# Kernel optimization log

Hardware: AMD Instinct MI355X
Metric: run time of the kernel (lower is better)

The kernel has to match this reference:

```python
import jax, jax.numpy as jnp
import numpy as np

B, N, C, H = 1, 4096, 768, 12
HD = C // H  # 64
EPS = 1e-5


def _rope_freqs(n, hd, theta=10000.0):
    inv = 1.0 / (theta ** (np.arange(0, hd, 2, dtype=np.float32) / hd))  # (hd/2,)
    ang = np.outer(np.arange(n, dtype=np.float32), inv)  # (N, hd/2)
    return jnp.asarray(np.cos(ang)), jnp.asarray(np.sin(ang))


def setup_inputs() -> dict:
    key = jax.random.key(0)
    ks = jax.random.split(key, 5)
    cos, sin = _rope_freqs(N, HD)
    s = lambda d: 1.0 / np.sqrt(d)
    return {
        "x": jax.random.normal(ks[0], (B, N, C), jnp.float32),
        "freqs_cos": cos,
        "freqs_sin": sin,
        "w_qkv": jax.random.normal(ks[1], (3 * C, C), jnp.float32) * s(C),
        "w_proj": jax.random.normal(ks[2], (C, C), jnp.float32) * s(C),
        "b_proj": jnp.zeros((C,), jnp.float32),
        "g1": jnp.ones((C,), jnp.float32),
        "beta1": jnp.zeros((C,), jnp.float32),
        "g2": jnp.ones((C,), jnp.float32),
        "beta2": jnp.zeros((C,), jnp.float32),
        "w_fc1": jax.random.normal(ks[3], (4 * C, C), jnp.float32) * s(C),
        "b_fc1": jnp.zeros((4 * C,), jnp.float32),
        "w_fc2": jax.random.normal(ks[4], (C, 4 * C), jnp.float32) * s(4 * C),
        "b_fc2": jnp.zeros((C,), jnp.float32),
    }


def _layernorm(x, g, b):
    mu = jnp.mean(x, -1, keepdims=True)
    var = jnp.mean(jnp.square(x - mu), -1, keepdims=True)
    return (x - mu) * jax.lax.rsqrt(var + EPS) * g + b


def _apply_rope(t, cos, sin):
    # t: (B, N, H, HD); cos/sin: (N, HD/2) -> broadcast (1, N, 1, HD/2)
    t = t.reshape(*t.shape[:-1], HD // 2, 2)
    t0, t1 = t[..., 0], t[..., 1]
    c = cos[None, :, None, :]
    s = sin[None, :, None, :]
    out = jnp.stack([t0 * c - t1 * s, t0 * s + t1 * c], axis=-1)
    return out.reshape(*out.shape[:-2], HD)


def reference(x, freqs_cos, freqs_sin, w_qkv, w_proj, b_proj, g1, beta1, g2, beta2,
              w_fc1, b_fc1, w_fc2, b_fc2):
    # --- attention branch ---
    h = _layernorm(x, g1, beta1)
    qkv = (h @ w_qkv.T).reshape(B, N, 3, H, HD)
    q, k, v = qkv[:, :, 0], qkv[:, :, 1], qkv[:, :, 2]  # (B,N,H,HD)
    q = _apply_rope(q, freqs_cos, freqs_sin)
    k = _apply_rope(k, freqs_cos, freqs_sin)
    scale = HD ** (-0.5)
    attn = jnp.einsum('bnhd,bmhd->bhnm', q, k) * scale
    attn = jax.nn.softmax(attn, axis=-1)
    o = jnp.einsum('bhnm,bmhd->bnhd', attn, v).reshape(B, N, C)
    x = x + o @ w_proj.T + b_proj
    # --- mlp branch ---
    h = _layernorm(x, g2, beta2)
    h = jax.nn.gelu(h @ w_fc1.T + b_fc1, approximate=False)
    x = x + h @ w_fc2.T + b_fc2
    return x
```

## Files before the change

kernel.cpp:

```cpp
#include <hip/hip_runtime.h>
#include <hip/hip_bf16.h>
#include <math.h>

#define LOG2E 1.44269504088896340736f

typedef short bf16x8 __attribute__((ext_vector_type(8)));
typedef float f32x4 __attribute__((ext_vector_type(4)));

static __device__ __forceinline__ float bf2f(ushort u){
  union { float f; unsigned int u; } x; x.u = ((unsigned int)u) << 16; return x.f;
}
static __device__ __forceinline__ ushort f2bf(float f){
  union { float f; unsigned int u; } x; x.f = f;
  unsigned int r = x.u + 0x7fffu + ((x.u >> 16) & 1u);
  return (ushort)(r >> 16);
}
static __device__ __forceinline__ unsigned cvt_pk_bf16(float a, float b){
  unsigned r;
  asm("v_cvt_pk_bf16_f32 %0, %1, %2" : "=v"(r) : "v"(a), "v"(b));
  return r;
}
static __device__ __forceinline__ float fmax3(float a, float b, float c){
  return fmaxf(fmaxf(a, b), c);
}
static __device__ __forceinline__ float dpp_xor1(float v){
  int i = __builtin_amdgcn_mov_dpp(__float_as_int(v), 0xB1, 0xF, 0xF, true);
  return __int_as_float(i);
}
static __device__ __forceinline__ void gload_lds16(const void* g, void* l){
  __builtin_amdgcn_global_load_lds(
      (const __attribute__((address_space(1))) unsigned int*)g,
      (__attribute__((address_space(3))) unsigned int*)l, 16, 0, 0);
}

__global__ __launch_bounds__(256) void cvt_all(const float* __restrict__ s0, ushort* __restrict__ d0, int c0,
                                               const float* __restrict__ s1, ushort* __restrict__ d1, int c1,
                                               const float* __restrict__ s2, ushort* __restrict__ d2, int c2,
                                               const float* __restrict__ s3, ushort* __restrict__ d3, int c3){
  int j = blockIdx.x * 256 + threadIdx.x;
  const float* s; ushort* d;
  if (j < c0){ s = s0; d = d0; }
  else { j -= c0;
    if (j < c1){ s = s1; d = d1; }
    else { j -= c1;
      if (j < c2){ s = s2; d = d2; }
      else { j -= c2; if (j >= c3) return; s = s3; d = d3; } } }
  float4 v = ((const float4*)s)[j];
  ushort4 o;
  o.x = f2bf(v.x); o.y = f2bf(v.y); o.z = f2bf(v.z); o.w = f2bf(v.w);
  ((ushort4*)d)[j] = o;
}

__global__ __launch_bounds__(256) void ln_kernel(const float* __restrict__ x,
                                                 const float* __restrict__ g,
                                                 const float* __restrict__ bta,
                                                 ushort* __restrict__ out){
  int w = threadIdx.x >> 6, l = threadIdx.x & 63;
  int row = blockIdx.x * 4 + w;
  const float* xr = x + (size_t)row * 768;
  f32x4 v[3];
  #pragma unroll
  for (int i = 0; i < 3; ++i) v[i] = *(const f32x4*)(xr + i * 256 + l * 4);
  float s = 0.0f;
  #pragma unroll
  for (int i = 0; i < 3; ++i)
    #pragma unroll
    for (int r = 0; r < 4; ++r) s += v[i][r];
  #pragma unroll
  for (int off = 32; off; off >>= 1) s += __shfl_xor(s, off, 64);
  float mu = s * (1.0f / 768.0f);
  float q = 0.0f;
  #pragma unroll
  for (int i = 0; i < 3; ++i)
    #pragma unroll
    for (int r = 0; r < 4; ++r){ float d = v[i][r] - mu; q += d * d; }
  #pragma unroll
  for (int off = 32; off; off >>= 1) q += __shfl_xor(q, off, 64);
  float rs = rsqrtf(q * (1.0f / 768.0f) + 1e-5f);
  ushort* orow = out + (size_t)row * 768;
  #pragma unroll
  for (int i = 0; i < 3; ++i){
    f32x4 gg = *(const f32x4*)(g + i * 256 + l * 4);
    f32x4 bb = *(const f32x4*)(bta + i * 256 + l * 4);
    ushort4 o;
    o.x = f2bf((v[i][0] - mu) * rs * gg[0] + bb[0]);
    o.y = f2bf((v[i][1] - mu) * rs * gg[1] + bb[1]);
    o.z = f2bf((v[i][2] - mu) * rs * gg[2] + bb[2]);
    o.w = f2bf((v[i][3] - mu) * rs * gg[3] + bb[3]);
    *(ushort4*)(orow + i * 256 + l * 4) = o;
  }
}

template<int MODE>
__global__ __launch_bounds__(256) void gemm_bf16(const ushort* __restrict__ A, int lda,
                                                 const ushort* __restrict__ Bm, int ldb,
                                                 int K,
                                                 const float* __restrict__ bias,
                                                 const float* __restrict__ res, int ldr,
                                                 void* __restrict__ out, int ldo,
                                                 const float* __restrict__ fc,
                                                 const float* __restrict__ fs,
                                                 ushort* __restrict__ Qs,
                                                 ushort* __restrict__ Ks,
                                                 ushort* __restrict__ Vt){
  __shared__ __align__(16) ushort As[128 * 64];
  __shared__ __align__(16) ushort Bs[128 * 64];
  const int tid = threadIdx.x;
  const int m0 = blockIdx.x * 128, n0 = blockIdx.y * 128;
  const int w = tid >> 6, l = tid & 63;
  const int wm = (w >> 1) * 64, wn = (w & 1) * 64;
  const int lr = l & 15, lg = l >> 4;
  const int lane8 = l >> 3, sl = l & 7;
  const int koff = (MODE == 3) ? blockIdx.z * K : 0;

  f32x4 acc[4][4] = {};

  for (int k0 = 0; k0 < K; k0 += 64){
    #pragma unroll
    for (int j = 0; j < 4; ++j){
      int instr = w * 4 + j;
      int row = instr * 8 + lane8;
      gload_lds16((const char*)A + ((size_t)(m0 + row) * lda + koff + k0) * 2 + ((sl ^ (row & 7)) << 4),
                  (char*)As + instr * 1024);
      gload_lds16((const char*)Bm + ((size_t)(n0 + row) * ldb + koff + k0) * 2 + ((sl ^ (row & 7)) << 4),
                  (char*)Bs + instr * 1024);
    }
    __syncthreads();
    #pragma unroll
    for (int kk = 0; kk < 2; ++kk){
      bf16x8 af[4], bfr[4];
      #pragma unroll
      for (int mi = 0; mi < 4; ++mi){
        int row = wm + mi * 16 + lr;
        int cg = (kk * 4 + lg) ^ (row & 7);
        af[mi] = *(const bf16x8*)(As + row * 64 + cg * 8);
      }
      #pragma unroll
      for (int nj = 0; nj < 4; ++nj){
        int row = wn + nj * 16 + lr;
        int cg = (kk * 4 + lg) ^ (row & 7);
        bfr[nj] = *(const bf16x8*)(Bs + row * 64 + cg * 8);
      }
      #pragma unroll
      for (int mi = 0; mi < 4; ++mi)
        #pragma unroll
        for (int nj = 0; nj < 4; ++nj)
          acc[mi][nj] = __builtin_amdgcn_mfma_f32_16x16x32_bf16(af[mi], bfr[nj], acc[mi][nj], 0, 0, 0);
    }
    __syncthreads();
  }

  const size_t zout = (MODE == 3) ? (size_t)blockIdx.z * gridDim.x * 128 * ldo : 0;

  if (MODE == 4){
    const int part = n0 / 768;
    const float qsc = 0.125f * LOG2E;
    #pragma unroll
    for (int mi = 0; mi < 4; ++mi){
      const int n_base = m0 + wm + mi * 16 + lg * 4;
      #pragma unroll
      for (int nj = 0; nj < 4; ++nj){
        const int col = n0 + wn + nj * 16 + lr;
        const int head = (col - part * 768) >> 6;
        const int d = col & 63;
        if (part == 2){
          ushort4 pk;
          pk.x = f2bf(acc[mi][nj][0]); pk.y = f2bf(acc[mi][nj][1]);
          pk.z = f2bf(acc[mi][nj][2]); pk.w = f2bf(acc[mi][nj][3]);
          *(ushort4*)(Vt + ((size_t)head * 64 + d) * 4096 + n_base) = pk;
        } else {
          const int p = d >> 1;
          ushort* dst = (part == 0) ? Qs : Ks;
          #pragma unroll
          for (int r = 0; r < 4; ++r){
            int n = n_base + r;
            float v = acc[mi][nj][r];
            float pv = dpp_xor1(v);
            float c = fc[(size_t)n * 32 + p];
            float sv = fs[(size_t)n * 32 + p];
            float rr = v * c + pv * ((d & 1) ? sv : -sv);
            if (part == 0) rr *= qsc;
            dst[((size_t)head * 4096 + n) * 64 + d] = f2bf(rr);
          }
        }
      }
    }
    return;
  }

  #pragma unroll
  for (int mi = 0; mi < 4; ++mi){
    #pragma unroll
    for (int nj = 0; nj < 4; ++nj){
      #pragma unroll
      for (int r = 0; r < 4; ++r){
        int grow = m0 + wm + mi * 16 + lg * 4 + r;
        int gcol = n0 + wn + nj * 16 + lr;
        float v = acc[mi][nj][r];
        if (MODE == 0){
          ((ushort*)out)[(size_t)grow * ldo + gcol] = f2bf(v);
        } else if (MODE == 1){
          v += bias[gcol] + res[(size_t)grow * ldr + gcol];
          ((float*)out)[(size_t)grow * ldo + gcol] = v;
        } else if (MODE == 2){
          v += bias[gcol];
          v = 0.5f * v * (1.0f + erff(v * 0.70710678118654752f));
          ((ushort*)out)[(size_t)grow * ldo + gcol] = f2bf(v);
        } else {
          ((float*)out)[zout + (size_t)grow * ldo + gcol] = v;
        }
      }
    }
  }
}

__global__ __launch_bounds__(192) void gemm_combine4(const float* __restrict__ parts,
                                                     const float* __restrict__ bias,
                                                     const float* __restrict__ res,
                                                     float* __restrict__ out){
  int q = blockIdx.x, t = threadIdx.x;
  size_t idx = (size_t)q * 768 + t * 4;
  const size_t seg = (size_t)4096 * 768;
  f32x4 o = *(const f32x4*)(parts + idx);
  #pragma unroll
  for (int s = 1; s < 4; ++s) o += *(const f32x4*)(parts + s * seg + idx);
  f32x4 b = *(const f32x4*)(bias + t * 4);
  f32x4 rr = *(const f32x4*)(res + idx);
  o += b + rr;
  *(f32x4*)(out + idx) = o;
}

__global__ __launch_bounds__(256, 4) void flash_attn(const ushort* __restrict__ Qs,
                                                     const ushort* __restrict__ Ks,
                                                     const ushort* __restrict__ Vt,
                                                     float* __restrict__ Opart,
                                                     float* __restrict__ Ml){
  __shared__ __align__(16) char smem[32768];
  const int h = blockIdx.y, kh = blockIdx.z;
  const int w = threadIdx.x >> 6, l = threadIdx.x & 63;
  const int lr = l & 15, lg = l >> 4;
  const int lane8 = l >> 3, sl = l & 7;
  const int q0 = blockIdx.x * 128 + w * 32;
  const ushort* Qh = Qs + (size_t)h * (4096 * 64);
  const char* Kh = (const char*)(Ks + (size_t)h * (4096 * 64));
  const char* Vh = (const char*)(Vt + (size_t)h * (64 * 4096));

  bf16x8 qa[2][2];
  #pragma unroll
  for (int qf = 0; qf < 2; ++qf)
    #pragma unroll
    for (int kk = 0; kk < 2; ++kk)
      qa[qf][kk] = *(const bf16x8*)(Qh + (size_t)(q0 + qf * 16 + lr) * 64 + kk * 32 + lg * 8);

  const char* kbase = Kh + (size_t)(kh * 1024 + w * 16 + lane8) * 128;
  const char* vbase = Vh + (size_t)(w * 16 + lane8) * 8192 + kh * 2048 + ((sl ^ lane8) << 4);
  int koff[2];
  #pragma unroll
  for (int j = 0; j < 2; ++j)
    koff[j] = j * 1024 + ((sl ^ ((lane8 & 3) | (((w * 2 + j) & 1) << 2))) << 4);

  const int a_ = lr >> 2, b_ = lr & 3;
  const int krow = 8 * a_ + b_;
  const int f_ = b_ | ((a_ & 1) << 2);
  const int kslot0 = (lg ^ f_) << 4;
  const int kslot1 = ((4 + lg) ^ f_) << 4;
  const int vslot0 = lr * 128 + ((lg ^ (lr & 7)) << 4);
  const int vslot1 = lr * 128 + (((4 + lg) ^ (lr & 7)) << 4);

  f32x4 oacc[2][4] = {};
  f32x4 lacc[2] = {};
  float m_prev[2] = {0.0f, 0.0f};
  union { unsigned u[4]; bf16x8 v; } ones;
  #pragma unroll
  for (int i = 0; i < 4; ++i) ones.u[i] = 0x3F803F80u;

  auto stage = [&](int tile, char* Kb, char* Vb){
    #pragma unroll
    for (int j = 0; j < 2; ++j){
      gload_lds16(kbase + (size_t)tile * 8192 + koff[j], Kb + (w * 2 + j) * 1024);
      gload_lds16(vbase + (size_t)j * 65536 + (size_t)tile * 128, Vb + (w * 2 + j) * 1024);
    }
  };

  auto compute = [&](const char* Kb, const char* Vb, bool first){
    f32x4 sh[2][4];
    #pragma unroll
    for (int qf = 0; qf < 2; ++qf){
      float iv = first ? 0.0f : -m_prev[qf];
      #pragma unroll
      for (int t = 0; t < 4; ++t){
        sh[qf][t][0] = iv; sh[qf][t][1] = iv; sh[qf][t][2] = iv; sh[qf][t][3] = iv;
      }
    }
    #pragma unroll
    for (int t = 0; t < 4; ++t){
      const char* kr = Kb + (krow + 4 * (t & 1) + 32 * (t >> 1)) * 128;
      bf16x8 k0 = *(const bf16x8*)(kr + kslot0);
      bf16x8 k1 = *(const bf16x8*)(kr + kslot1);
      #pragma unroll
      for (int qf = 0; qf < 2; ++qf){
        sh[qf][t] = __builtin_amdgcn_mfma_f32_16x16x32_bf16(k0, qa[qf][0], sh[qf][t], 0, 0, 0);
        sh[qf][t] = __builtin_amdgcn_mfma_f32_16x16x32_bf16(k1, qa[qf][1], sh[qf][t], 0, 0, 0);
      }
    }
    float mb[2];
    #pragma unroll
    for (int qf = 0; qf < 2; ++qf){
      float m1 = fmax3(sh[qf][0][0], sh[qf][0][1], sh[qf][0][2]);
      float m2 = fmax3(sh[qf][0][3], sh[qf][1][0], sh[qf][1][1]);
      float m3 = fmax3(sh[qf][1][2], sh[qf][1][3], sh[qf][2][0]);
      float m4 = fmax3(sh[qf][2][1], sh[qf][2][2], sh[qf][2][3]);
      float m5 = fmax3(sh[qf][3][0], sh[qf][3][1], sh[qf][3][2]);
      mb[qf] = fmax3(fmaxf(m1, m2), fmax3(m3, m4, m5), sh[qf][3][3]);
    }
    if (first){
      #pragma unroll
      for (int qf = 0; qf < 2; ++qf){
        float mm = fmaxf(mb[qf], __shfl_xor(mb[qf], 16, 64));
        mm = fmaxf(mm, __shfl_xor(mm, 32, 64));
        m_prev[qf] = mm;
        #pragma unroll
        for (int t = 0; t < 4; ++t)
          #pragma unroll
          for (int r = 0; r < 4; ++r) sh[qf][t][r] -= mm;
      }
    } else if (!__all(mb[0] <= 8.0f && mb[1] <= 8.0f)){
      #pragma unroll
      for (int qf = 0; qf < 2; ++qf){
        float mm = fmaxf(mb[qf], __shfl_xor(mb[qf], 16, 64));
        mm = fmaxf(mm, __shfl_xor(mm, 32, 64));
        float d = (mm > 8.0f) ? mm : 0.0f;
        float sc = exp2f(-d);
        #pragma unroll
        for (int t = 0; t < 4; ++t)
          #pragma unroll
          for (int r = 0; r < 4; ++r) sh[qf][t][r] -= d;
        #pragma unroll
        for (int db = 0; db < 4; ++db)
          #pragma unroll
          for (int r = 0; r < 4; ++r) oacc[qf][db][r] *= sc;
        #pragma unroll
        for (int r = 0; r < 4; ++r) lacc[qf][r] *= sc;
        m_prev[qf] += d;
      }
    }
    #pragma unroll
    for (int qf = 0; qf < 2; ++qf)
      #pragma unroll
      for (int t = 0; t < 4; ++t)
        #pragma unroll
        for (int r = 0; r < 4; ++r)
          sh[qf][t][r] = exp2f(sh[qf][t][r]);
    #pragma unroll
    for (int kk = 0; kk < 2; ++kk){
      union { unsigned u[4]; bf16x8 v; } pf[2];
      #pragma unroll
      for (int qf = 0; qf < 2; ++qf){
        pf[qf].u[0] = cvt_pk_bf16(sh[qf][2*kk][0],   sh[qf][2*kk][1]);
        pf[qf].u[1] = cvt_pk_bf16(sh[qf][2*kk][2],   sh[qf][2*kk][3]);
        pf[qf].u[2] = cvt_pk_bf16(sh[qf][2*kk+1][0], sh[qf][2*kk+1][1]);
        pf[qf].u[3] = cvt_pk_bf16(sh[qf][2*kk+1][2], sh[qf][2*kk+1][3]);
      }
      const int vs = kk ? vslot1 : vslot0;
      #pragma unroll
      for (int db = 0; db < 4; ++db){
        bf16x8 vf = *(const bf16x8*)(Vb + vs + db * 2048);
        #pragma unroll
        for (int qf = 0; qf < 2; ++qf)
          oacc[qf][db] = __builtin_amdgcn_mfma_f32_16x16x32_bf16(vf, pf[qf].v, oacc[qf][db], 0, 0, 0);
      }
      #pragma unroll
      for (int qf = 0; qf < 2; ++qf)
        lacc[qf] = __builtin_amdgcn_mfma_f32_16x16x32_bf16(ones.v, pf[qf].v, lacc[qf], 0, 0, 0);
    }
  };

  char* K0 = smem;          char* V0 = smem + 8192;
  char* K1 = smem + 16384;  char* V1 = smem + 24576;

  stage(0, K0, V0);
  __syncthreads();
  stage(1, K1, V1);
  compute(K0, V0, true);
  __syncthreads();
  stage(2, K0, V0);
  compute(K1, V1, false);
  __syncthreads();
  #pragma unroll 1
  for (int it2 = 1; it2 < 8; ++it2){
    stage(2 * it2 + 1, K1, V1);
    compute(K0, V0, false);
    __syncthreads();
    if (it2 < 7) stage(2 * it2 + 2, K0, V0);
    compute(K1, V1, false);
    __syncthreads();
  }

  #pragma unroll
  for (int qf = 0; qf < 2; ++qf){
    int q = q0 + qf * 16 + lr;
    float* Op = Opart + ((size_t)(kh * 12 + h) * 4096 + q) * 64;
    #pragma unroll
    for (int db = 0; db < 4; ++db)
      *(f32x4*)(Op + db * 16 + 4 * lg) = oacc[qf][db];
    if (lg == 0){
      float2 ml; ml.x = m_prev[qf]; ml.y = lacc[qf][0];
      *(float2*)(Ml + ((size_t)(kh * 12 + h) * 4096 + q) * 2) = ml;
    }
  }
}

__global__ __launch_bounds__(192) void attn_combine(const float* __restrict__ Opart,
                                                    const float* __restrict__ Ml,
                                                    ushort* __restrict__ O){
  int q = blockIdx.x, t = threadIdx.x;
  int h = t >> 4;
  float2 ml[4];
  float m = -1e30f;
  #pragma unroll
  for (int s = 0; s < 4; ++s){
    ml[s] = *(const float2*)(Ml + ((size_t)(s * 12 + h) * 4096 + q) * 2);
    m = fmaxf(m, ml[s].x);
  }
  float wgt[4], lsum = 0.0f;
  #pragma unroll
  for (int s = 0; s < 4; ++s){
    wgt[s] = exp2f(ml[s].x - m);
    lsum += ml[s].y * wgt[s];
  }
  float inv = 1.0f / lsum;
  int dd = (t & 15) * 4;
  f32x4 o = {};
  #pragma unroll
  for (int s = 0; s < 4; ++s){
    f32x4 os = *(const f32x4*)(Opart + ((size_t)(s * 12 + h) * 4096 + q) * 64 + dd);
    #pragma unroll
    for (int r = 0; r < 4; ++r) o[r] += os[r] * wgt[s];
  }
  uint2 ov;
  ov.x = cvt_pk_bf16(o[0] * inv, o[1] * inv);
  ov.y = cvt_pk_bf16(o[2] * inv, o[3] * inv);
  *(uint2*)(O + (size_t)q * 768 + t * 4) = ov;
}

extern "C" void kernel_launch(void* const* d_in, const int* in_sizes, int n_in,
                              void* d_out, int out_size, void* d_ws, size_t ws_size,
                              hipStream_t stream){
  const float* x      = (const float*)d_in[0];
  const float* fcos   = (const float*)d_in[1];
  const float* fsin   = (const float*)d_in[2];
  const float* w_qkv  = (const float*)d_in[3];
  const float* w_proj = (const float*)d_in[4];
  const float* b_proj = (const float*)d_in[5];
  const float* g1     = (const float*)d_in[6];
  const float* beta1  = (const float*)d_in[7];
  const float* g2     = (const float*)d_in[8];
  const float* beta2  = (const float*)d_in[9];
  const float* w_fc1  = (const float*)d_in[10];
  const float* b_fc1  = (const float*)d_in[11];
  const float* w_fc2  = (const float*)d_in[12];
  const float* b_fc2  = (const float*)d_in[13];

  char* ws = (char*)d_ws;
  size_t off = 0;
  auto alloc = [&](size_t bytes) -> char* {
    char* p = ws + off; off += (bytes + 255) & ~(size_t)255; return p;
  };
  ushort* wq  = (ushort*)alloc((size_t)2304 * 768 * 2);
  ushort* wp  = (ushort*)alloc((size_t)768 * 768 * 2);
  ushort* w1  = (ushort*)alloc((size_t)3072 * 768 * 2);
  ushort* w2  = (ushort*)alloc((size_t)768 * 3072 * 2);
  ushort* h1  = (ushort*)alloc((size_t)4096 * 768 * 2);
  ushort* Qs  = (ushort*)alloc((size_t)12 * 4096 * 64 * 2);
  ushort* Ks  = (ushort*)alloc((size_t)12 * 4096 * 64 * 2);
  ushort* Vt  = (ushort*)alloc((size_t)12 * 64 * 4096 * 2);
  ushort* ao  = (ushort*)alloc((size_t)4096 * 768 * 2);
  float*  x2  = (float*) alloc((size_t)4096 * 768 * 4);
  ushort* h2  = (ushort*)alloc((size_t)4096 * 768 * 2);
  ushort* f1  = (ushort*)alloc((size_t)4096 * 3072 * 2);
  float*  Opart = (float*)alloc((size_t)4 * 12 * 4096 * 64 * 4);
  float*  Ml    = (float*)alloc((size_t)4 * 12 * 4096 * 2 * 4);
  float*  skp   = Opart;

  const int c0 = 2304*768/4, c1 = 768*768/4, c2 = 3072*768/4, c3 = 768*3072/4;
  cvt_all<<<(c0 + c1 + c2 + c3 + 255)/256, 256, 0, stream>>>(
      w_qkv, wq, c0, w_proj, wp, c1, w_fc1, w1, c2, w_fc2, w2, c3);

  ln_kernel<<<1024, 256, 0, stream>>>(x, g1, beta1, h1);
  gemm_bf16<4><<<dim3(32, 18), 256, 0, stream>>>(h1, 768, wq, 768, 768,
                                                 nullptr, nullptr, 0, nullptr, 0,
                                                 fcos, fsin, Qs, Ks, Vt);
  flash_attn<<<dim3(32, 12, 4), 256, 0, stream>>>(Qs, Ks, Vt, Opart, Ml);
  attn_combine<<<4096, 192, 0, stream>>>(Opart, Ml, ao);
  gemm_bf16<1><<<dim3(32, 6), 256, 0, stream>>>(ao, 768, wp, 768, 768,
                                                b_proj, x, 768, x2, 768,
                                                nullptr, nullptr, nullptr, nullptr, nullptr);
  ln_kernel<<<1024, 256, 0, stream>>>(x2, g2, beta2, h2);
  gemm_bf16<2><<<dim3(32, 24), 256, 0, stream>>>(h2, 768, w1, 768, 768,
                                                 b_fc1, nullptr, 0, f1, 3072,
                                                 nullptr, nullptr, nullptr, nullptr, nullptr);
  gemm_bf16<3><<<dim3(32, 6, 4), 256, 0, stream>>>(f1, 3072, w2, 3072, 768,
                                                   nullptr, nullptr, 0, skp, 768,
                                                   nullptr, nullptr, nullptr, nullptr, nullptr);
  gemm_combine4<<<4096, 192, 0, stream>>>(skp, b_fc2, x2, (float*)d_out);
}
```

Measured before the change: 244.1 us.

## Replace 128x128 four-wave GEMM with single-wave 64x64 tile kernel without barriers

The GEMM kernel now runs one wave per block on a 64x64 output tile instead of four waves on a 128x128 tile. Since a single wave owns the whole tile, __syncthreads is replaced by explicit s_waitcnt vmcnt/lgkmcnt waits. The grid gets four times as many blocks and shared memory per block drops, aiming at higher occupancy and no barrier stalls on this fairly small problem. In exchange, each element loaded is reused less (half the tile width), so global and LDS traffic per FLOP goes up, and each wave's loads are exposed with no overlap from other waves in the same block.

Result: no change. 248.6 us (+1.8%).

```diff
diff --git a/kernel.cpp b/kernel.cpp
--- a/kernel.cpp
+++ b/kernel.cpp
@@ -92,52 +92,53 @@
 }
 
 template<int MODE>
-__global__ __launch_bounds__(256) void gemm_bf16(const ushort* __restrict__ A, int lda,
-                                                 const ushort* __restrict__ Bm, int ldb,
-                                                 int K,
-                                                 const float* __restrict__ bias,
-                                                 const float* __restrict__ res, int ldr,
-                                                 void* __restrict__ out, int ldo,
-                                                 const float* __restrict__ fc,
-                                                 const float* __restrict__ fs,
-                                                 ushort* __restrict__ Qs,
-                                                 ushort* __restrict__ Ks,
-                                                 ushort* __restrict__ Vt){
-  __shared__ __align__(16) ushort As[128 * 64];
-  __shared__ __align__(16) ushort Bs[128 * 64];
-  const int tid = threadIdx.x;
-  const int m0 = blockIdx.x * 128, n0 = blockIdx.y * 128;
-  const int w = tid >> 6, l = tid & 63;
-  const int wm = (w >> 1) * 64, wn = (w & 1) * 64;
+__global__ __launch_bounds__(64) void gemm64(const ushort* __restrict__ A, int lda,
+                                             const ushort* __restrict__ Bm, int ldb,
+                                             int K,
+                                             const float* __restrict__ bias,
+                                             const float* __restrict__ res, int ldr,
+                                             void* __restrict__ out, int ldo,
+                                             const float* __restrict__ fc,
+                                             const float* __restrict__ fs,
+                                             ushort* __restrict__ Qs,
+                                             ushort* __restrict__ Ks,
+                                             ushort* __restrict__ Vt){
+  __shared__ __align__(16) ushort As[64 * 64];
+  __shared__ __align__(16) ushort Bs[64 * 64];
+  const int l = threadIdx.x;
+  const int m0 = blockIdx.x * 64, n0 = blockIdx.y * 64;
   const int lr = l & 15, lg = l >> 4;
   const int lane8 = l >> 3, sl = l & 7;
   const int koff = (MODE == 3) ? blockIdx.z * K : 0;
 
   f32x4 acc[4][4] = {};
 
-  for (int k0 = 0; k0 < K; k0 += 64){
-    #pragma unroll
-    for (int j = 0; j < 4; ++j){
-      int instr = w * 4 + j;
-      int row = instr * 8 + lane8;
+  const int nk = K >> 6;
+  #pragma unroll 1
+  for (int ki = 0; ki < nk; ++ki){
+    const int k0 = ki << 6;
+    asm volatile("s_waitcnt lgkmcnt(0)" ::: "memory");
+    #pragma unroll
+    for (int j = 0; j < 8; ++j){
+      int row = j * 8 + lane8;
       gload_lds16((const char*)A + ((size_t)(m0 + row) * lda + koff + k0) * 2 + ((sl ^ (row & 7)) << 4),
-                  (char*)As + instr * 1024);
+                  (char*)As + j * 1024);
       gload_lds16((const char*)Bm + ((size_t)(n0 + row) * ldb + koff + k0) * 2 + ((sl ^ (row & 7)) << 4),
-                  (char*)Bs + instr * 1024);
-    }
-    __syncthreads();
+                  (char*)Bs + j * 1024);
+    }
+    asm volatile("s_waitcnt vmcnt(0)" ::: "memory");
     #pragma unroll
     for (int kk = 0; kk < 2; ++kk){
       bf16x8 af[4], bfr[4];
       #pragma unroll
       for (int mi = 0; mi < 4; ++mi){
-        int row = wm + mi * 16 + lr;
+        int row = mi * 16 + lr;
         int cg = (kk * 4 + lg) ^ (row & 7);
         af[mi] = *(const bf16x8*)(As + row * 64 + cg * 8);
       }
       #pragma unroll
       for (int nj = 0; nj < 4; ++nj){
-        int row = wn + nj * 16 + lr;
+        int row = nj * 16 + lr;
         int cg = (kk * 4 + lg) ^ (row & 7);
         bfr[nj] = *(const bf16x8*)(Bs + row * 64 + cg * 8);
       }
@@ -147,20 +148,19 @@
         for (int nj = 0; nj < 4; ++nj)
           acc[mi][nj] = __builtin_amdgcn_mfma_f32_16x16x32_bf16(af[mi], bfr[nj], acc[mi][nj], 0, 0, 0);
     }
-    __syncthreads();
-  }
-
-  const size_t zout = (MODE == 3) ? (size_t)blockIdx.z * gridDim.x * 128 * ldo : 0;
+  }
+
+  const size_t zout = (MODE == 3) ? (size_t)blockIdx.z * 4096 * ldo : 0;
 
   if (MODE == 4){
     const int part = n0 / 768;
     const float qsc = 0.125f * LOG2E;
     #pragma unroll
     for (int mi = 0; mi < 4; ++mi){
-      const int n_base = m0 + wm + mi * 16 + lg * 4;
+      const int n_base = m0 + mi * 16 + lg * 4;
       #pragma unroll
       for (int nj = 0; nj < 4; ++nj){
-        const int col = n0 + wn + nj * 16 + lr;
+        const int col = n0 + nj * 16 + lr;
         const int head = (col - part * 768) >> 6;
         const int d = col & 63;
         if (part == 2){
@@ -194,8 +194,8 @@
     for (int nj = 0; nj < 4; ++nj){
       #pragma unroll
       for (int r = 0; r < 4; ++r){
-        int grow = m0 + wm + mi * 16 + lg * 4 + r;
-        int gcol = n0 + wn + nj * 16 + lr;
+        int grow = m0 + mi * 16 + lg * 4 + r;
+        int gcol = n0 + nj * 16 + lr;
         float v = acc[mi][nj][r];
         if (MODE == 0){
           ((ushort*)out)[(size_t)grow * ldo + gcol] = f2bf(v);
@@ -487,20 +487,20 @@
       w_qkv, wq, c0, w_proj, wp, c1, w_fc1, w1, c2, w_fc2, w2, c3);
 
   ln_kernel<<<1024, 256, 0, stream>>>(x, g1, beta1, h1);
-  gemm_bf16<4><<<dim3(32, 18), 256, 0, stream>>>(h1, 768, wq, 768, 768,
-                                                 nullptr, nullptr, 0, nullptr, 0,
-                                                 fcos, fsin, Qs, Ks, Vt);
+  gemm64<4><<<dim3(64, 36), 64, 0, stream>>>(h1, 768, wq, 768, 768,
+                                             nullptr, nullptr, 0, nullptr, 0,
+                                             fcos, fsin, Qs, Ks, Vt);
   flash_attn<<<dim3(32, 12, 4), 256, 0, stream>>>(Qs, Ks, Vt, Opart, Ml);
   attn_combine<<<4096, 192, 0, stream>>>(Opart, Ml, ao);
-  gemm_bf16<1><<<dim3(32, 6), 256, 0, stream>>>(ao, 768, wp, 768, 768,
-                                                b_proj, x, 768, x2, 768,
+  gemm64<1><<<dim3(64, 12), 64, 0, stream>>>(ao, 768, wp, 768, 768,
+                                             b_proj, x, 768, x2, 768,
+                                             nullptr, nullptr, nullptr, nullptr, nullptr);
+  ln_kernel<<<1024, 256, 0, stream>>>(x2, g2, beta2, h2);
+  gemm64<2><<<dim3(64, 48), 64, 0, stream>>>(h2, 768, w1, 768, 768,
+                                             b_fc1, nullptr, 0, f1, 3072,
+                                             nullptr, nullptr, nullptr, nullptr, nullptr);
+  gemm64<3><<<dim3(64, 12, 4), 64, 0, stream>>>(f1, 3072, w2, 3072, 768,
+                                                nullptr, nullptr, 0, skp, 768,
                                                 nullptr, nullptr, nullptr, nullptr, nullptr);
-  ln_kernel<<<1024, 256, 0, stream>>>(x2, g2, beta2, h2);
-  gemm_bf16<2><<<dim3(32, 24), 256, 0, stream>>>(h2, 768, w1, 768, 768,
-                                                 b_fc1, nullptr, 0, f1, 3072,
-                                                 nullptr, nullptr, nullptr, nullptr, nullptr);
-  gemm_bf16<3><<<dim3(32, 6, 4), 256, 0, stream>>>(f1, 3072, w2, 3072, 768,
-                                                   nullptr, nullptr, 0, skp, 768,
-                                                   nullptr, nullptr, nullptr, nullptr, nullptr);
   gemm_combine4<<<4096, 192, 0, stream>>>(skp, b_fc2, x2, (float*)d_out);
 }
```
